# Performance work log

Measured on AMD Instinct MI355X. Metric: run time of the kernel, lower is better.

Reference implementation:

```python
import jax, jax.numpy as jnp
import numpy as np

NUM_GRAPHS = 128
NODES_PER_GRAPH = 512
LATENT_DIM = 256


def setup_inputs() -> dict:
    key = jax.random.key(0)
    n_total = NUM_GRAPHS * NODES_PER_GRAPH
    z = jax.random.normal(key, (n_total, LATENT_DIM), dtype=jnp.float32)
    # sorted graph assignment: nodes of graph i are contiguous
    batch = (jnp.arange(n_total, dtype=jnp.int32) // NODES_PER_GRAPH).astype(jnp.int32)
    return {"z": z, "batch": batch, "num_graphs": NUM_GRAPHS, "max_nodes": NODES_PER_GRAPH}


def reference(z, batch, num_graphs, max_nodes):
    # Eval-mode forward (dropout is identity when not training).
    n_total, d = z.shape
    ones = jnp.ones((n_total,), dtype=jnp.int32)
    counts = jax.ops.segment_sum(ones, batch, num_segments=num_graphs)  # [G]
    starts = jnp.concatenate([jnp.zeros((1,), jnp.int32), jnp.cumsum(counts)[:-1].astype(jnp.int32)])
    pos = jnp.arange(n_total, dtype=jnp.int32) - starts[batch]  # intra-graph node index
    # Scatter nodes into zero-padded [G, max_nodes, D] tensor
    z_pad = jnp.zeros((num_graphs, max_nodes, d), dtype=z.dtype).at[batch, pos].set(z)
    valid = jnp.zeros((num_graphs, max_nodes), dtype=bool).at[batch, pos].set(True)
    # Per-graph inner-product decoder + sigmoid, padded positions forced to 0
    adj = jax.nn.sigmoid(jnp.einsum('gnd,gmd->gnm', z_pad, z_pad))  # [G, N, N]
    mask = valid[:, :, None] & valid[:, None, :]
    return jnp.where(mask, adj, jnp.zeros((), dtype=adj.dtype))
```

## Files before the change

### kernel.cpp

```cpp
#include <hip/hip_runtime.h>

typedef __fp16 fp16x2 __attribute__((ext_vector_type(2)));
typedef _Float16 half8 __attribute__((ext_vector_type(8)));
typedef float floatx4 __attribute__((ext_vector_type(4)));

namespace {

constexpr int NODES = 512;
constexpr int DIM   = 256;
constexpr int BM    = 128;
constexpr int BK    = 64;

union Cvt8 { fp16x2 h2[4]; half8 h8; };

__device__ inline half8 pack8(const floatx4 f0, const floatx4 f1) {
  Cvt8 c;
  c.h2[0] = __builtin_amdgcn_cvt_pkrtz(f0.x, f0.y);
  c.h2[1] = __builtin_amdgcn_cvt_pkrtz(f0.z, f0.w);
  c.h2[2] = __builtin_amdgcn_cvt_pkrtz(f1.x, f1.y);
  c.h2[3] = __builtin_amdgcn_cvt_pkrtz(f1.z, f1.w);
  return c.h8;
}

__device__ inline half8 pack8(const float4 f0, const float4 f1) {
  Cvt8 c;
  c.h2[0] = __builtin_amdgcn_cvt_pkrtz(f0.x, f0.y);
  c.h2[1] = __builtin_amdgcn_cvt_pkrtz(f0.z, f0.w);
  c.h2[2] = __builtin_amdgcn_cvt_pkrtz(f1.x, f1.y);
  c.h2[3] = __builtin_amdgcn_cvt_pkrtz(f1.z, f1.w);
  return c.h8;
}

__device__ inline void async_ld16(const void* g, void* lds) {
  __builtin_amdgcn_global_load_lds(
      (const __attribute__((address_space(1))) unsigned int*)g,
      (__attribute__((address_space(3))) unsigned int*)lds,
      16, 0, 0);
}

__device__ inline float sigmoidf(float x) {
  return __builtin_amdgcn_rcpf(1.0f + __expf(-x));
}

__global__ __launch_bounds__(256)
void cvt_kernel(const float* __restrict__ z, _Float16* __restrict__ z16) {
  const int b = blockIdx.x;
  const int x = b & 7;
  const int j = b >> 3;
  const int g = x + 8 * (j >> 6);
  const int chunk = j & 63;
  const size_t base = ((size_t)g * NODES + (size_t)chunk * 8) * DIM
                    + (size_t)threadIdx.x * 8;
  const floatx4* p = reinterpret_cast<const floatx4*>(z + base);
  const floatx4 f0 = __builtin_nontemporal_load(p);
  const floatx4 f1 = __builtin_nontemporal_load(p + 1);
  *reinterpret_cast<half8*>(z16 + base) = pack8(f0, f1);
}

__global__ __launch_bounds__(256, 4)
void gemm_kernel(const _Float16* __restrict__ z16, float* __restrict__ out) {
  __shared__ __align__(16) _Float16 As[BM * BK];
  __shared__ __align__(16) _Float16 Bs[BM * BK];

  const int bid = blockIdx.x;
  const int x    = bid & 7;
  const int j    = bid >> 3;
  const int ggrp = j / 10;
  const int t    = j - ggrp * 10;
  const int g    = x + 8 * ggrp;

  int tn, tm;
  if (t < 4)      { tn = 0; tm = t; }
  else if (t < 7) { tn = 1; tm = t - 3; }
  else if (t < 9) { tn = 2; tm = t - 5; }
  else            { tn = 3; tm = 3; }
  const bool diag = (tn == tm);

  const int tid  = threadIdx.x;
  const int lane = tid & 63;
  const int wave = tid >> 6;
  const int wRow = wave >> 1;
  const int wCol = wave & 1;
  const int lrow = lane & 15;
  const int quad = lane >> 4;

  const _Float16* zA = z16 + ((size_t)g * NODES + tn * BM) * DIM;
  const _Float16* zB = z16 + ((size_t)g * NODES + tm * BM) * DIM;

  const int sRow = lane >> 3;
  const int sCp  = (lane & 7) ^ sRow;
  const size_t sOffH = (size_t)sRow * DIM + sCp * 8;

  const _Float16* Bsrc = diag ? As : Bs;

  floatx4 acc[4][4];
#pragma unroll
  for (int i = 0; i < 4; ++i)
#pragma unroll
    for (int jj = 0; jj < 4; ++jj)
      acc[i][jj] = (floatx4){0.f, 0.f, 0.f, 0.f};

  for (int kk = 0; kk < DIM; kk += BK) {
#pragma unroll
    for (int it = 0; it < 4; ++it) {
      const int q = wave * 4 + it;
      const _Float16* gA = zA + (size_t)q * 8 * DIM + kk + sOffH;
      async_ld16(gA, &As[q * 512]);
      if (!diag) {
        const _Float16* gB = zB + (size_t)q * 8 * DIM + kk + sOffH;
        async_ld16(gB, &Bs[q * 512]);
      }
    }
    __syncthreads();

#pragma unroll
    for (int ks = 0; ks < 2; ++ks) {
      half8 af[4], bf[4];
#pragma unroll
      for (int i = 0; i < 4; ++i) {
        const int row = wRow * 64 + i * 16 + lrow;
        const int cp = (ks * 4 + quad) ^ (lrow & 7);
        af[i] = *reinterpret_cast<const half8*>(&As[row * BK + cp * 8]);
      }
#pragma unroll
      for (int jj = 0; jj < 4; ++jj) {
        const int row = wCol * 64 + jj * 16 + lrow;
        const int cp = (ks * 4 + quad) ^ (lrow & 7);
        bf[jj] = *reinterpret_cast<const half8*>(&Bsrc[row * BK + cp * 8]);
      }
#pragma unroll
      for (int i = 0; i < 4; ++i)
#pragma unroll
        for (int jj = 0; jj < 4; ++jj)
          acc[i][jj] = __builtin_amdgcn_mfma_f32_16x16x32_f16(af[i], bf[jj], acc[i][jj], 0, 0, 0);
    }
    __syncthreads();
  }

  float* outg = out + (size_t)g * NODES * NODES;
  const int nBase = tn * BM + wRow * 64;
  const int mBase = tm * BM + wCol * 64;
#pragma unroll
  for (int jj = 0; jj < 4; ++jj) {
    const int m = mBase + jj * 16 + lrow;
    float* rowp = outg + (size_t)m * NODES;
#pragma unroll
    for (int i = 0; i < 4; ++i) {
      const int n0 = nBase + i * 16 + quad * 4;
      floatx4 v;
#pragma unroll
      for (int r = 0; r < 4; ++r)
        v[r] = sigmoidf(acc[i][jj][r]);
      *reinterpret_cast<floatx4*>(rowp + n0) = v;
      if (!diag) {
#pragma unroll
        for (int r = 0; r < 4; ++r)
          outg[(size_t)(n0 + r) * NODES + m] = v[r];
      }
    }
  }
}

constexpr int LSTR = 72;
__global__ __launch_bounds__(256, 4)
void fallback_kernel(const float* __restrict__ z, float* __restrict__ out) {
  __shared__ _Float16 As[BM * LSTR];
  __shared__ _Float16 Bs[BM * LSTR];
  const int bid = blockIdx.x;
  const int g    = (bid & 7) + 8 * (bid >> 7);
  const int tile = (bid >> 3) & 15;
  const int tn   = tile >> 2;
  const int tm   = tile & 3;
  const int tid  = threadIdx.x;
  const int lane = tid & 63;
  const int wave = tid >> 6;
  const int wRow = wave >> 1;
  const int wCol = wave & 1;
  const int lrow = lane & 15;
  const int quad = lane >> 4;
  const float* zA = z + ((size_t)g * NODES + tn * BM) * DIM;
  const float* zB = z + ((size_t)g * NODES + tm * BM) * DIM;
  const int srow  = tid >> 1;
  const int shalf = tid & 1;
  floatx4 acc[4][4];
#pragma unroll
  for (int i = 0; i < 4; ++i)
#pragma unroll
    for (int j = 0; j < 4; ++j)
      acc[i][j] = (floatx4){0.f, 0.f, 0.f, 0.f};
  for (int kk = 0; kk < DIM; kk += BK) {
    {
      const float4* pa = reinterpret_cast<const float4*>(zA + srow * DIM + kk + shalf * 32);
      _Float16* da = &As[srow * LSTR + shalf * 32];
      float4 f0 = pa[0], f1 = pa[1], f2 = pa[2], f3 = pa[3];
      *reinterpret_cast<half8*>(da)     = pack8(f0, f1);
      *reinterpret_cast<half8*>(da + 8) = pack8(f2, f3);
      f0 = pa[4]; f1 = pa[5]; f2 = pa[6]; f3 = pa[7];
      *reinterpret_cast<half8*>(da + 16) = pack8(f0, f1);
      *reinterpret_cast<half8*>(da + 24) = pack8(f2, f3);
    }
    {
      const float4* pb = reinterpret_cast<const float4*>(zB + srow * DIM + kk + shalf * 32);
      _Float16* db = &Bs[srow * LSTR + shalf * 32];
      float4 f0 = pb[0], f1 = pb[1], f2 = pb[2], f3 = pb[3];
      *reinterpret_cast<half8*>(db)     = pack8(f0, f1);
      *reinterpret_cast<half8*>(db + 8) = pack8(f2, f3);
      f0 = pb[4]; f1 = pb[5]; f2 = pb[6]; f3 = pb[7];
      *reinterpret_cast<half8*>(db + 16) = pack8(f0, f1);
      *reinterpret_cast<half8*>(db + 24) = pack8(f2, f3);
    }
    __syncthreads();
#pragma unroll
    for (int ks = 0; ks < 2; ++ks) {
      half8 af[4], bf[4];
#pragma unroll
      for (int i = 0; i < 4; ++i)
        af[i] = *reinterpret_cast<const half8*>(
            &As[(wRow * 64 + i * 16 + lrow) * LSTR + ks * 32 + quad * 8]);
#pragma unroll
      for (int j = 0; j < 4; ++j)
        bf[j] = *reinterpret_cast<const half8*>(
            &Bs[(wCol * 64 + j * 16 + lrow) * LSTR + ks * 32 + quad * 8]);
#pragma unroll
      for (int i = 0; i < 4; ++i)
#pragma unroll
        for (int j = 0; j < 4; ++j)
          acc[i][j] = __builtin_amdgcn_mfma_f32_16x16x32_f16(af[i], bf[j], acc[i][j], 0, 0, 0);
    }
    __syncthreads();
  }
  float* outg = out + (size_t)g * NODES * NODES;
  const int nBase = tn * BM + wRow * 64;
  const int mBase = tm * BM + wCol * 64;
#pragma unroll
  for (int i = 0; i < 4; ++i) {
#pragma unroll
    for (int j = 0; j < 4; ++j) {
      const int m = mBase + j * 16 + lrow;
#pragma unroll
      for (int r = 0; r < 4; ++r) {
        const int n = nBase + i * 16 + quad * 4 + r;
        const float x = acc[i][j][r];
        outg[(size_t)n * NODES + m] = sigmoidf(x);
      }
    }
  }
}

}

extern "C" void kernel_launch(void* const* d_in, const int* in_sizes, int n_in,
                              void* d_out, int out_size, void* d_ws, size_t ws_size,
                              hipStream_t stream) {
  const float* z = (const float*)d_in[0];
  float* out = (float*)d_out;
  const size_t need = (size_t)128 * 512 * 256 * sizeof(_Float16);
  if (ws_size >= need) {
    _Float16* z16 = (_Float16*)d_ws;
    hipLaunchKernelGGL(cvt_kernel, dim3(8192), dim3(256), 0, stream, z, z16);
    hipLaunchKernelGGL(gemm_kernel, dim3(128 * 10), dim3(256), 0, stream, z16, out);
  } else {
    hipLaunchKernelGGL(fallback_kernel, dim3(128 * 16), dim3(256), 0, stream, z, out);
  }
}
```

Before: 229.7 us.

## Fuse fp32-to-fp16 conversion into GEMM by staging fp32 tiles in LDS

Removes the separate conversion kernel and workspace buffer; the GEMM now async-loads fp32 tiles into swizzled LDS and converts to fp16 fragments right before the MFMAs. This eliminates an extra pass over the input and a kernel launch. In exchange, LDS usage doubles, occupancy is lowered to 2 blocks per CU, global read volume for the GEMM doubles, and conversion instructions are repeated per tile reuse. The fallback path is dropped.

```diff
diff --git a/kernel.cpp b/kernel.cpp
--- a/kernel.cpp
+++ b/kernel.cpp
@@ -9,20 +9,11 @@
 constexpr int NODES = 512;
 constexpr int DIM   = 256;
 constexpr int BM    = 128;
-constexpr int BK    = 64;
+constexpr int BKF   = 64;
 
 union Cvt8 { fp16x2 h2[4]; half8 h8; };
 
 __device__ inline half8 pack8(const floatx4 f0, const floatx4 f1) {
-  Cvt8 c;
-  c.h2[0] = __builtin_amdgcn_cvt_pkrtz(f0.x, f0.y);
-  c.h2[1] = __builtin_amdgcn_cvt_pkrtz(f0.z, f0.w);
-  c.h2[2] = __builtin_amdgcn_cvt_pkrtz(f1.x, f1.y);
-  c.h2[3] = __builtin_amdgcn_cvt_pkrtz(f1.z, f1.w);
-  return c.h8;
-}
-
-__device__ inline half8 pack8(const float4 f0, const float4 f1) {
   Cvt8 c;
   c.h2[0] = __builtin_amdgcn_cvt_pkrtz(f0.x, f0.y);
   c.h2[1] = __builtin_amdgcn_cvt_pkrtz(f0.z, f0.w);
@@ -42,25 +33,10 @@
   return __builtin_amdgcn_rcpf(1.0f + __expf(-x));
 }
 
-__global__ __launch_bounds__(256)
-void cvt_kernel(const float* __restrict__ z, _Float16* __restrict__ z16) {
-  const int b = blockIdx.x;
-  const int x = b & 7;
-  const int j = b >> 3;
-  const int g = x + 8 * (j >> 6);
-  const int chunk = j & 63;
-  const size_t base = ((size_t)g * NODES + (size_t)chunk * 8) * DIM
-                    + (size_t)threadIdx.x * 8;
-  const floatx4* p = reinterpret_cast<const floatx4*>(z + base);
-  const floatx4 f0 = __builtin_nontemporal_load(p);
-  const floatx4 f1 = __builtin_nontemporal_load(p + 1);
-  *reinterpret_cast<half8*>(z16 + base) = pack8(f0, f1);
-}
-
-__global__ __launch_bounds__(256, 4)
-void gemm_kernel(const _Float16* __restrict__ z16, float* __restrict__ out) {
-  __shared__ __align__(16) _Float16 As[BM * BK];
-  __shared__ __align__(16) _Float16 Bs[BM * BK];
+__global__ __launch_bounds__(256, 2)
+void fused_kernel(const float* __restrict__ z, float* __restrict__ out) {
+  __shared__ __align__(16) float As[BM * BKF];
+  __shared__ __align__(16) float Bs[BM * BKF];
 
   const int bid = blockIdx.x;
   const int x    = bid & 7;
@@ -84,14 +60,13 @@
   const int lrow = lane & 15;
   const int quad = lane >> 4;
 
-  const _Float16* zA = z16 + ((size_t)g * NODES + tn * BM) * DIM;
-  const _Float16* zB = z16 + ((size_t)g * NODES + tm * BM) * DIM;
+  const float* zA = z + ((size_t)g * NODES + tn * BM) * DIM;
+  const float* zB = z + ((size_t)g * NODES + tm * BM) * DIM;
 
-  const int sRow = lane >> 3;
-  const int sCp  = (lane & 7) ^ sRow;
-  const size_t sOffH = (size_t)sRow * DIM + sCp * 8;
+  const int sRowL = lane >> 4;
+  const int sC    = lane & 15;
 
-  const _Float16* Bsrc = diag ? As : Bs;
+  const float* Bsrc = diag ? As : Bs;
 
   floatx4 acc[4][4];
 #pragma unroll
@@ -100,33 +75,39 @@
     for (int jj = 0; jj < 4; ++jj)
       acc[i][jj] = (floatx4){0.f, 0.f, 0.f, 0.f};
 
-  for (int kk = 0; kk < DIM; kk += BK) {
+  for (int kk = 0; kk < DIM; kk += BKF) {
 #pragma unroll
-    for (int it = 0; it < 4; ++it) {
-      const int q = wave * 4 + it;
-      const _Float16* gA = zA + (size_t)q * 8 * DIM + kk + sOffH;
-      async_ld16(gA, &As[q * 512]);
-      if (!diag) {
-        const _Float16* gB = zB + (size_t)q * 8 * DIM + kk + sOffH;
-        async_ld16(gB, &Bs[q * 512]);
-      }
+    for (int it = 0; it < 8; ++it) {
+      const int q   = wave * 8 + it;
+      const int row = q * 4 + sRowL;
+      const int cs  = sC ^ (row & 15);
+      const size_t srcOff = (size_t)row * DIM + kk + cs * 4;
+      async_ld16(zA + srcOff, &As[q * 256]);
+      if (!diag) async_ld16(zB + srcOff, &Bs[q * 256]);
     }
     __syncthreads();
 
 #pragma unroll
     for (int ks = 0; ks < 2; ++ks) {
+      const int cg0 = ks * 8 + quad * 2;
       half8 af[4], bf[4];
 #pragma unroll
       for (int i = 0; i < 4; ++i) {
         const int row = wRow * 64 + i * 16 + lrow;
-        const int cp = (ks * 4 + quad) ^ (lrow & 7);
-        af[i] = *reinterpret_cast<const half8*>(&As[row * BK + cp * 8]);
+        const floatx4 a0 = *reinterpret_cast<const floatx4*>(
+            &As[row * BKF + ((cg0)     ^ lrow) * 4]);
+        const floatx4 a1 = *reinterpret_cast<const floatx4*>(
+            &As[row * BKF + ((cg0 + 1) ^ lrow) * 4]);
+        af[i] = pack8(a0, a1);
       }
 #pragma unroll
       for (int jj = 0; jj < 4; ++jj) {
         const int row = wCol * 64 + jj * 16 + lrow;
-        const int cp = (ks * 4 + quad) ^ (lrow & 7);
-        bf[jj] = *reinterpret_cast<const half8*>(&Bsrc[row * BK + cp * 8]);
+        const floatx4 b0 = *reinterpret_cast<const floatx4*>(
+            &Bsrc[row * BKF + ((cg0)     ^ lrow) * 4]);
+        const floatx4 b1 = *reinterpret_cast<const floatx4*>(
+            &Bsrc[row * BKF + ((cg0 + 1) ^ lrow) * 4]);
+        bf[jj] = pack8(b0, b1);
       }
 #pragma unroll
       for (int i = 0; i < 4; ++i)
@@ -161,92 +142,6 @@
   }
 }
 
-constexpr int LSTR = 72;
-__global__ __launch_bounds__(256, 4)
-void fallback_kernel(const float* __restrict__ z, float* __restrict__ out) {
-  __shared__ _Float16 As[BM * LSTR];
-  __shared__ _Float16 Bs[BM * LSTR];
-  const int bid = blockIdx.x;
-  const int g    = (bid & 7) + 8 * (bid >> 7);
-  const int tile = (bid >> 3) & 15;
-  const int tn   = tile >> 2;
-  const int tm   = tile & 3;
-  const int tid  = threadIdx.x;
-  const int lane = tid & 63;
-  const int wave = tid >> 6;
-  const int wRow = wave >> 1;
-  const int wCol = wave & 1;
-  const int lrow = lane & 15;
-  const int quad = lane >> 4;
-  const float* zA = z + ((size_t)g * NODES + tn * BM) * DIM;
-  const float* zB = z + ((size_t)g * NODES + tm * BM) * DIM;
-  const int srow  = tid >> 1;
-  const int shalf = tid & 1;
-  floatx4 acc[4][4];
-#pragma unroll
-  for (int i = 0; i < 4; ++i)
-#pragma unroll
-    for (int j = 0; j < 4; ++j)
-      acc[i][j] = (floatx4){0.f, 0.f, 0.f, 0.f};
-  for (int kk = 0; kk < DIM; kk += BK) {
-    {
-      const float4* pa = reinterpret_cast<const float4*>(zA + srow * DIM + kk + shalf * 32);
-      _Float16* da = &As[srow * LSTR + shalf * 32];
-      float4 f0 = pa[0], f1 = pa[1], f2 = pa[2], f3 = pa[3];
-      *reinterpret_cast<half8*>(da)     = pack8(f0, f1);
-      *reinterpret_cast<half8*>(da + 8) = pack8(f2, f3);
-      f0 = pa[4]; f1 = pa[5]; f2 = pa[6]; f3 = pa[7];
-      *reinterpret_cast<half8*>(da + 16) = pack8(f0, f1);
-      *reinterpret_cast<half8*>(da + 24) = pack8(f2, f3);
-    }
-    {
-      const float4* pb = reinterpret_cast<const float4*>(zB + srow * DIM + kk + shalf * 32);
-      _Float16* db = &Bs[srow * LSTR + shalf * 32];
-      float4 f0 = pb[0], f1 = pb[1], f2 = pb[2], f3 = pb[3];
-      *reinterpret_cast<half8*>(db)     = pack8(f0, f1);
-      *reinterpret_cast<half8*>(db + 8) = pack8(f2, f3);
-      f0 = pb[4]; f1 = pb[5]; f2 = pb[6]; f3 = pb[7];
-      *reinterpret_cast<half8*>(db + 16) = pack8(f0, f1);
-      *reinterpret_cast<half8*>(db + 24) = pack8(f2, f3);
-    }
-    __syncthreads();
-#pragma unroll
-    for (int ks = 0; ks < 2; ++ks) {
-      half8 af[4], bf[4];
-#pragma unroll
-      for (int i = 0; i < 4; ++i)
-        af[i] = *reinterpret_cast<const half8*>(
-            &As[(wRow * 64 + i * 16 + lrow) * LSTR + ks * 32 + quad * 8]);
-#pragma unroll
-      for (int j = 0; j < 4; ++j)
-        bf[j] = *reinterpret_cast<const half8*>(
-            &Bs[(wCol * 64 + j * 16 + lrow) * LSTR + ks * 32 + quad * 8]);
-#pragma unroll
-      for (int i = 0; i < 4; ++i)
-#pragma unroll
-        for (int j = 0; j < 4; ++j)
-          acc[i][j] = __builtin_amdgcn_mfma_f32_16x16x32_f16(af[i], bf[j], acc[i][j], 0, 0, 0);
-    }
-    __syncthreads();
-  }
-  float* outg = out + (size_t)g * NODES * NODES;
-  const int nBase = tn * BM + wRow * 64;
-  const int mBase = tm * BM + wCol * 64;
-#pragma unroll
-  for (int i = 0; i < 4; ++i) {
-#pragma unroll
-    for (int j = 0; j < 4; ++j) {
-      const int m = mBase + j * 16 + lrow;
-#pragma unroll
-      for (int r = 0; r < 4; ++r) {
-        const int n = nBase + i * 16 + quad * 4 + r;
-        const float x = acc[i][j][r];
-        outg[(size_t)n * NODES + m] = sigmoidf(x);
-      }
-    }
-  }
-}
-
 }
 
 extern "C" void kernel_launch(void* const* d_in, const int* in_sizes, int n_in,
@@ -254,12 +149,6 @@
                               hipStream_t stream) {
   const float* z = (const float*)d_in[0];
   float* out = (float*)d_out;
-  const size_t need = (size_t)128 * 512 * 256 * sizeof(_Float16);
-  if (ws_size >= need) {
-    _Float16* z16 = (_Float16*)d_ws;
-    hipLaunchKernelGGL(cvt_kernel, dim3(8192), dim3(256), 0, stream, z, z16);
-    hipLaunchKernelGGL(gemm_kernel, dim3(128 * 10), dim3(256), 0, stream, z16, out);
-  } else {
-    hipLaunchKernelGGL(fallback_kernel, dim3(128 * 16), dim3(256), 0, stream, z, out);
-  }
+  (void)d_ws; (void)ws_size;
+  hipLaunchKernelGGL(fused_kernel, dim3(128 * 10), dim3(256), 0, stream, z, out);
 }
```

After: 193.0 us. -16.0%, faster.
